# Performance work log

Measured on AMD Instinct MI355X. Metric: run time of the kernel, lower is better.

The kernel has to match this reference:

```python
import jax, jax.numpy as jnp
import numpy as np
import math

B, L1, L2, NHID, NH, HD = 4, 2048, 2048, 1024, 16, 64


def setup_inputs() -> dict:
    key = jax.random.key(0)
    ks = jax.random.split(key, 8)
    s = 1.0 / math.sqrt(NHID)  # keep activations O(1)
    inp1 = jax.random.normal(ks[0], (B, L1, NHID), dtype=jnp.float32)
    inp2 = jax.random.normal(ks[1], (B, L2, NHID), dtype=jnp.float32)
    mask = jnp.zeros((B, L2), dtype=bool)
    Wq = jax.random.normal(ks[2], (NHID, NH * HD), dtype=jnp.float32) * s
    Wk = jax.random.normal(ks[3], (NHID, NH * HD), dtype=jnp.float32) * s
    Wv = jax.random.normal(ks[4], (NHID, NH * HD), dtype=jnp.float32) * s
    Wo = jax.random.normal(ks[5], (NH * HD, NHID), dtype=jnp.float32) * s
    bq = jnp.zeros((NH * HD,), jnp.float32)
    bk = jnp.zeros((NH * HD,), jnp.float32)
    bv = jnp.zeros((NH * HD,), jnp.float32)
    bo = jnp.zeros((NHID,), jnp.float32)
    return dict(inp1=inp1, inp2=inp2, mask=mask, Wq=Wq, bq=bq, Wk=Wk, bk=bk,
                Wv=Wv, bv=bv, Wo=Wo, bo=bo)


def reference(inp1, inp2, mask, Wq, bq, Wk, bk, Wv, bv, Wo, bo):
    # q/k/v projections
    q = (inp1 @ Wq + bq) / math.sqrt(HD)              # [B,L1,NH*HD]
    k = inp2 @ Wk + bk                                 # [B,L2,NH*HD]
    v = inp2 @ Wv + bv                                 # [B,L2,NH*HD]
    q = q.reshape(B, L1, NH, HD)
    k = k.reshape(B, L2, NH, HD)
    v = v.reshape(B, L2, NH, HD)
    # scores [B,NH,L1,L2]
    scores = jnp.einsum('bqhd,bkhd->bhqk', q, k)
    scores = jnp.where(mask[:, None, None, :], jnp.float32(-1e8), scores)
    alpha = jax.nn.softmax(scores, axis=-1)
    attn = jnp.einsum('bhqk,bkhd->bqhd', alpha, v).reshape(B, L1, NH * HD)
    return attn @ Wo + bo                              # [B,L1,NHID]
```

## Files before the change

kernel.cpp:

```cpp
#include <hip/hip_runtime.h>
#include <hip/hip_bf16.h>
#include <stdint.h>

using f32x4  = __attribute__((ext_vector_type(4))) float;
using bf16x8 = __attribute__((ext_vector_type(8))) __bf16;

__device__ __forceinline__ unsigned short f2bf(float f) {
  union { float f; unsigned u; } x; x.f = f;
  unsigned r = x.u + 0x7fffu + ((x.u >> 16) & 1u);
  return (unsigned short)(r >> 16);
}

__device__ __forceinline__ void gload_lds16(const void* g, void* l) {
  __builtin_amdgcn_global_load_lds((const __attribute__((address_space(1))) void*)g,
                                   (__attribute__((address_space(3))) void*)l, 16, 0, 0);
}

__global__ __launch_bounds__(256) void f32_to_bf16_k(const float* __restrict__ in,
                                                     unsigned short* __restrict__ out, int n4) {
  int i = blockIdx.x * 256 + threadIdx.x;
  if (i >= n4) return;
  const float4 v = *(const float4*)(in + (size_t)i * 4);
  union { unsigned short s[4]; uint2 u; } p;
  p.s[0] = f2bf(v.x); p.s[1] = f2bf(v.y); p.s[2] = f2bf(v.z); p.s[3] = f2bf(v.w);
  *(uint2*)(out + (size_t)i * 4) = p.u;
}

__global__ __launch_bounds__(256) void prep_wt_k(const float* __restrict__ W,
                                                 unsigned short* __restrict__ WT, float scale) {
  __shared__ float t[32][33];
  const int tx = threadIdx.x & 31, ty = threadIdx.x >> 5;
  const int gx = blockIdx.x * 32, gy = blockIdx.y * 32;
  #pragma unroll
  for (int r = ty; r < 32; r += 8) t[r][tx] = W[(size_t)(gy + r) * 1024 + gx + tx];
  __syncthreads();
  #pragma unroll
  for (int r = ty; r < 32; r += 8)
    WT[(size_t)(gx + r) * 1024 + gy + tx] = f2bf(t[tx][r] * scale);
}

template<int EPI>
__global__ __launch_bounds__(256) void gemm_bt_k(
    const unsigned short* __restrict__ A,
    const unsigned short* __restrict__ BT,
    const float* __restrict__ bias, float bias_scale,
    void* __restrict__ Cv,
    int M, int N, int K) {
  constexpr int BM = 128, BN = 128, BK = 64;
  __shared__ unsigned short sA[BM * BK];
  __shared__ unsigned short sB[BN * BK];
  const int tid = threadIdx.x;
  const int w = tid >> 6, l = tid & 63, l15 = l & 15, lhi = l >> 4;
  const int wr = w >> 1, wc = w & 1;
  const int m0 = blockIdx.y * BM, n0 = blockIdx.x * BN;

  const f32x4 zero = {0.f, 0.f, 0.f, 0.f};
  f32x4 acc[4][4];
  #pragma unroll
  for (int i = 0; i < 4; i++)
    #pragma unroll
    for (int j = 0; j < 4; j++) acc[i][j] = zero;

  for (int k0 = 0; k0 < K; k0 += BK) {
    __syncthreads();
    #pragma unroll
    for (int i = 0; i < 4; i++) {
      const int p = tid + i * 256;
      const int row = p >> 3;
      const int cl = (p & 7) ^ (row & 7);
      gload_lds16(A + (size_t)(m0 + row) * K + k0 + cl * 8, sA + p * 8);
      gload_lds16(BT + (size_t)(n0 + row) * K + k0 + cl * 8, sB + p * 8);
    }
    __syncthreads();
    #pragma unroll
    for (int kk = 0; kk < 2; kk++) {
      bf16x8 af[4], bfr[4];
      #pragma unroll
      for (int mi = 0; mi < 4; mi++) {
        const int row = wr * 64 + mi * 16 + l15;
        const int c = (kk * 4 + lhi) ^ (row & 7);
        af[mi] = *(const bf16x8*)(sA + row * 64 + c * 8);
      }
      #pragma unroll
      for (int ni = 0; ni < 4; ni++) {
        const int row = wc * 64 + ni * 16 + l15;
        const int c = (kk * 4 + lhi) ^ (row & 7);
        bfr[ni] = *(const bf16x8*)(sB + row * 64 + c * 8);
      }
      #pragma unroll
      for (int mi = 0; mi < 4; mi++)
        #pragma unroll
        for (int ni = 0; ni < 4; ni++)
          acc[mi][ni] = __builtin_amdgcn_mfma_f32_16x16x32_bf16(af[mi], bfr[ni], acc[mi][ni], 0, 0, 0);
    }
  }
  #pragma unroll
  for (int mi = 0; mi < 4; mi++) {
    const int gr = m0 + wr * 64 + mi * 16 + lhi * 4;
    #pragma unroll
    for (int ni = 0; ni < 4; ni++) {
      const int gc = n0 + wc * 64 + ni * 16 + l15;
      const float bs = bias[gc] * bias_scale;
      if constexpr (EPI == 0) {
        unsigned short* C = (unsigned short*)Cv;
        #pragma unroll
        for (int j = 0; j < 4; j++)
          C[(size_t)(gr + j) * N + gc] = f2bf(acc[mi][ni][j] + bs);
      } else if constexpr (EPI == 1) {
        unsigned short* C = (unsigned short*)Cv;
        const int bb = gr >> 11, l2 = gr & 2047;
        const int hh = gc >> 6, dd = gc & 63;
        union { unsigned short s[4]; uint2 u; } pk;
        #pragma unroll
        for (int j = 0; j < 4; j++) pk.s[j] = f2bf(acc[mi][ni][j] + bs);
        *(uint2*)(C + ((size_t)((bb * 16 + hh) * 64 + dd) * 2048 + l2)) = pk.u;
      } else {
        float* C = (float*)Cv;
        #pragma unroll
        for (int j = 0; j < 4; j++)
          C[(size_t)(gr + j) * N + gc] = acc[mi][ni][j] + bs;
      }
    }
  }
}

__global__ __launch_bounds__(256, 3) void flash_k(
    const unsigned short* __restrict__ qb,
    const unsigned short* __restrict__ kb,
    const unsigned short* __restrict__ vTb,
    const unsigned char* __restrict__ mask,
    unsigned short* __restrict__ attnb) {
  __shared__ unsigned short sK[2][64 * 64];
  __shared__ unsigned short sV[2][64 * 64];
  __shared__ unsigned short sP[4][2][16 * 64];
  const int tid = threadIdx.x;
  const int w = tid >> 6, l = tid & 63, l15 = l & 15, lhi = l >> 4;
  const int id = blockIdx.x;
  const int xcd = id & 7;
  const int qt = (id >> 3) & 15;
  const int hb = ((id >> 7) << 3) + xcd;
  const int h = hb & 15, b = hb >> 4;

  const size_t qrowA = (size_t)(b * 2048 + qt * 128 + w * 16 + l15);
  const size_t qrowB = qrowA + 64;
  const bf16x8 aqA0 = *(const bf16x8*)(qb + qrowA * 1024 + h * 64 + lhi * 8);
  const bf16x8 aqA1 = *(const bf16x8*)(qb + qrowA * 1024 + h * 64 + 32 + lhi * 8);
  const bf16x8 aqB0 = *(const bf16x8*)(qb + qrowB * 1024 + h * 64 + lhi * 8);
  const bf16x8 aqB1 = *(const bf16x8*)(qb + qrowB * 1024 + h * 64 + 32 + lhi * 8);

  const f32x4 zero = {0.f, 0.f, 0.f, 0.f};
  f32x4 oaccA[5], oaccB[5];
  #pragma unroll
  for (int d = 0; d < 5; d++) { oaccA[d] = zero; oaccB[d] = zero; }
  float mrowA[4], mrowB[4];
  #pragma unroll
  for (int j = 0; j < 4; j++) { mrowA[j] = 8.0f; mrowB[j] = 8.0f; }

  bf16x8 onef;
  #pragma unroll
  for (int i = 0; i < 8; i++) onef[i] = (__bf16)1.0f;

  const unsigned short* kbase = kb + (size_t)(b * 2048) * 1024 + h * 64;
  const unsigned short* vbase = vTb + (size_t)((b * 16 + h) * 64) * 2048;
  const unsigned char* mbase = mask + b * 2048;
  unsigned short* sPA = sP[w][0];
  unsigned short* sPB = sP[w][1];

  bool anym_lane = false;
  for (int i = l; i < 2048; i += 64) anym_lane |= (mbase[i] != 0);
  const bool anym = __any(anym_lane);

  const int p0 = tid, p1 = tid + 256;
  const int r0 = p0 >> 3, c0s = (p0 & 7) ^ (r0 & 7);
  const int r1 = p1 >> 3, c1s = (p1 & 7) ^ (r1 & 7);
  const unsigned short* kp0 = kbase + (size_t)r0 * 1024 + c0s * 8;
  const unsigned short* kp1 = kbase + (size_t)r1 * 1024 + c1s * 8;
  const unsigned short* vp0 = vbase + (size_t)r0 * 2048 + c0s * 8;
  const unsigned short* vp1 = vbase + (size_t)r1 * 2048 + c1s * 8;

  gload_lds16(kp0, sK[0] + p0 * 8);
  gload_lds16(kp1, sK[0] + p1 * 8);
  gload_lds16(vp0, sV[0] + p0 * 8);
  gload_lds16(vp1, sV[0] + p1 * 8);
  __syncthreads();

  int cur = 0;
  for (int kt = 0; kt < 32; kt++) {
    if (kt < 31) {
      const size_t ko = (size_t)(kt + 1) * 64 * 1024;
      const int vo = (kt + 1) * 64;
      unsigned short* dK = sK[cur ^ 1];
      unsigned short* dV = sV[cur ^ 1];
      gload_lds16(kp0 + ko, dK + p0 * 8);
      gload_lds16(kp1 + ko, dK + p1 * 8);
      gload_lds16(vp0 + vo, dV + p0 * 8);
      gload_lds16(vp1 + vo, dV + p1 * 8);
    }
    const unsigned short* cK = sK[cur];
    const unsigned short* cV = sV[cur];

    f32x4 sA[4], sB[4];
    #pragma unroll
    for (int n = 0; n < 4; n++) { sA[n] = zero; sB[n] = zero; }
    #pragma unroll
    for (int n = 0; n < 4; n++) {
      const int row = n * 16 + l15;
      const int cc0 = lhi ^ (row & 7);
      const int cc1 = (4 + lhi) ^ (row & 7);
      const bf16x8 k0 = *(const bf16x8*)(cK + row * 64 + cc0 * 8);
      const bf16x8 k1 = *(const bf16x8*)(cK + row * 64 + cc1 * 8);
      sA[n] = __builtin_amdgcn_mfma_f32_16x16x32_bf16(aqA0, k0, sA[n], 0, 0, 0);
      sA[n] = __builtin_amdgcn_mfma_f32_16x16x32_bf16(aqA1, k1, sA[n], 0, 0, 0);
      sB[n] = __builtin_amdgcn_mfma_f32_16x16x32_bf16(aqB0, k0, sB[n], 0, 0, 0);
      sB[n] = __builtin_amdgcn_mfma_f32_16x16x32_bf16(aqB1, k1, sB[n], 0, 0, 0);
    }

    if (anym) {
      #pragma unroll
      for (int n = 0; n < 4; n++) {
        const float mb = mbase[kt * 64 + n * 16 + l15] ? -1e8f : 0.f;
        #pragma unroll
        for (int j = 0; j < 4; j++) { sA[n][j] += mb; sB[n][j] += mb; }
      }
    }

    {
      float lmax[4];
      #pragma unroll
      for (int j = 0; j < 4; j++)
        lmax[j] = fmaxf(fmaxf(sA[0][j], sA[1][j]), fmaxf(sA[2][j], sA[3][j]));
      const bool need = (lmax[0] > mrowA[0]) | (lmax[1] > mrowA[1]) |
                        (lmax[2] > mrowA[2]) | (lmax[3] > mrowA[3]);
      if (__any(need)) {
        float tmax[4] = {lmax[0], lmax[1], lmax[2], lmax[3]};
        #pragma unroll
        for (int d = 1; d < 16; d <<= 1)
          #pragma unroll
          for (int j = 0; j < 4; j++) tmax[j] = fmaxf(tmax[j], __shfl_xor(tmax[j], d));
        #pragma unroll
        for (int j = 0; j < 4; j++) {
          const float mnew = fmaxf(mrowA[j], tmax[j]);
          const float scl = exp2f(mrowA[j] - mnew);
          mrowA[j] = mnew;
          #pragma unroll
          for (int d = 0; d < 5; d++) oaccA[d][j] *= scl;
        }
      }
    }
    {
      float lmax[4];
      #pragma unroll
      for (int j = 0; j < 4; j++)
        lmax[j] = fmaxf(fmaxf(sB[0][j], sB[1][j]), fmaxf(sB[2][j], sB[3][j]));
      const bool need = (lmax[0] > mrowB[0]) | (lmax[1] > mrowB[1]) |
                        (lmax[2] > mrowB[2]) | (lmax[3] > mrowB[3]);
      if (__any(need)) {
        float tmax[4] = {lmax[0], lmax[1], lmax[2], lmax[3]};
        #pragma unroll
        for (int d = 1; d < 16; d <<= 1)
          #pragma unroll
          for (int j = 0; j < 4; j++) tmax[j] = fmaxf(tmax[j], __shfl_xor(tmax[j], d));
        #pragma unroll
        for (int j = 0; j < 4; j++) {
          const float mnew = fmaxf(mrowB[j], tmax[j]);
          const float scl = exp2f(mrowB[j] - mnew);
          mrowB[j] = mnew;
          #pragma unroll
          for (int d = 0; d < 5; d++) oaccB[d][j] *= scl;
        }
      }
    }

    #pragma unroll
    for (int n = 0; n < 4; n++)
      #pragma unroll
      for (int j = 0; j < 4; j++) {
        const int row = lhi * 4 + j;
        const int col = n * 16 + l15;
        const int cc = (col >> 3) ^ (row & 7);
        *(__bf16*)(sPA + row * 64 + cc * 8 + (col & 7)) = (__bf16)exp2f(sA[n][j] - mrowA[j]);
        *(__bf16*)(sPB + row * 64 + cc * 8 + (col & 7)) = (__bf16)exp2f(sB[n][j] - mrowB[j]);
      }
    asm volatile("s_waitcnt lgkmcnt(0)" ::: "memory");
    __builtin_amdgcn_sched_barrier(0);
    {
      const int prow = l15;
      const int pc0 = lhi ^ (prow & 7);
      const int pc1 = (4 + lhi) ^ (prow & 7);
      const bf16x8 paA0 = *(const bf16x8*)(sPA + prow * 64 + pc0 * 8);
      const bf16x8 paA1 = *(const bf16x8*)(sPA + prow * 64 + pc1 * 8);
      const bf16x8 paB0 = *(const bf16x8*)(sPB + prow * 64 + pc0 * 8);
      const bf16x8 paB1 = *(const bf16x8*)(sPB + prow * 64 + pc1 * 8);
      #pragma unroll
      for (int df = 0; df < 4; df++) {
        const int row = df * 16 + l15;
        const int cc0 = lhi ^ (row & 7);
        const int cc1 = (4 + lhi) ^ (row & 7);
        const bf16x8 v0 = *(const bf16x8*)(cV + row * 64 + cc0 * 8);
        const bf16x8 v1 = *(const bf16x8*)(cV + row * 64 + cc1 * 8);
        oaccA[df] = __builtin_amdgcn_mfma_f32_16x16x32_bf16(paA0, v0, oaccA[df], 0, 0, 0);
        oaccA[df] = __builtin_amdgcn_mfma_f32_16x16x32_bf16(paA1, v1, oaccA[df], 0, 0, 0);
        oaccB[df] = __builtin_amdgcn_mfma_f32_16x16x32_bf16(paB0, v0, oaccB[df], 0, 0, 0);
        oaccB[df] = __builtin_amdgcn_mfma_f32_16x16x32_bf16(paB1, v1, oaccB[df], 0, 0, 0);
      }
      oaccA[4] = __builtin_amdgcn_mfma_f32_16x16x32_bf16(paA0, onef, oaccA[4], 0, 0, 0);
      oaccA[4] = __builtin_amdgcn_mfma_f32_16x16x32_bf16(paA1, onef, oaccA[4], 0, 0, 0);
      oaccB[4] = __builtin_amdgcn_mfma_f32_16x16x32_bf16(paB0, onef, oaccB[4], 0, 0, 0);
      oaccB[4] = __builtin_amdgcn_mfma_f32_16x16x32_bf16(paB1, onef, oaccB[4], 0, 0, 0);
    }
    __syncthreads();
    cur ^= 1;
  }

  float invA[4], invB[4];
  #pragma unroll
  for (int j = 0; j < 4; j++) { invA[j] = 1.0f / oaccA[4][j]; invB[j] = 1.0f / oaccB[4][j]; }
  #pragma unroll
  for (int df = 0; df < 4; df++)
    #pragma unroll
    for (int j = 0; j < 4; j++) {
      const size_t rA = (size_t)(b * 2048 + qt * 128 + w * 16 + lhi * 4 + j);
      attnb[rA * 1024 + h * 64 + df * 16 + l15] = f2bf(oaccA[df][j] * invA[j]);
      attnb[(rA + 64) * 1024 + h * 64 + df * 16 + l15] = f2bf(oaccB[df][j] * invB[j]);
    }
}

extern "C" void kernel_launch(void* const* d_in, const int* in_sizes, int n_in,
                              void* d_out, int out_size, void* d_ws, size_t ws_size,
                              hipStream_t stream) {
  (void)in_sizes; (void)n_in; (void)out_size; (void)ws_size;
  const float* inp1 = (const float*)d_in[0];
  const float* inp2 = (const float*)d_in[1];
  const unsigned char* mask = (const unsigned char*)d_in[2];
  const float* Wq = (const float*)d_in[3];
  const float* bq = (const float*)d_in[4];
  const float* Wk = (const float*)d_in[5];
  const float* bk = (const float*)d_in[6];
  const float* Wv = (const float*)d_in[7];
  const float* bv = (const float*)d_in[8];
  const float* Wo = (const float*)d_in[9];
  const float* bo = (const float*)d_in[10];
  float* out = (float*)d_out;

  char* p = (char*)d_ws;
  auto alloc = [&](size_t bytes) { char* r = p; p += (bytes + 255) & ~(size_t)255; return r; };
  const size_t ACT = 8192ull * 1024 * 2;
  const size_t WSZ = 1024ull * 1024 * 2;
  unsigned short* x1b  = (unsigned short*)alloc(ACT);
  unsigned short* x2b  = (unsigned short*)alloc(ACT);
  unsigned short* WqT  = (unsigned short*)alloc(WSZ);
  unsigned short* WkT  = (unsigned short*)alloc(WSZ);
  unsigned short* WvT  = (unsigned short*)alloc(WSZ);
  unsigned short* WoT  = (unsigned short*)alloc(WSZ);
  unsigned short* qbuf = (unsigned short*)alloc(ACT);
  unsigned short* kbuf = (unsigned short*)alloc(ACT);
  unsigned short* vTbf = (unsigned short*)alloc(ACT);
  unsigned short* attb = x1b;

  const float QS = 0.18033688011112042f;

  f32_to_bf16_k<<<8192, 256, 0, stream>>>(inp1, x1b, 2097152);
  f32_to_bf16_k<<<8192, 256, 0, stream>>>(inp2, x2b, 2097152);
  dim3 tg(32, 32);
  prep_wt_k<<<tg, 256, 0, stream>>>(Wq, WqT, QS);
  prep_wt_k<<<tg, 256, 0, stream>>>(Wk, WkT, 1.f);
  prep_wt_k<<<tg, 256, 0, stream>>>(Wv, WvT, 1.f);
  prep_wt_k<<<tg, 256, 0, stream>>>(Wo, WoT, 1.f);
  dim3 gg(8, 64);
  gemm_bt_k<0><<<gg, 256, 0, stream>>>(x1b, WqT, bq, QS, qbuf, 8192, 1024, 1024);
  gemm_bt_k<0><<<gg, 256, 0, stream>>>(x2b, WkT, bk, 1.f, kbuf, 8192, 1024, 1024);
  gemm_bt_k<1><<<gg, 256, 0, stream>>>(x2b, WvT, bv, 1.f, vTbf, 8192, 1024, 1024);
  flash_k<<<1024, 256, 0, stream>>>(qbuf, kbuf, vTbf, mask, attb);
  gemm_bt_k<2><<<gg, 256, 0, stream>>>(attb, WoT, bo, 1.f, out, 8192, 1024, 1024);
}
```

Measured before the change: 276.4 us.

## Fuse K/V projection GEMMs, merge input conversions, and halve flash P scratch

The two input f32-to-bf16 conversion launches become one kernel, and the K and V projection GEMMs become a single N=2048 GEMM whose epilogue writes K row-major and V transposed. In the flash kernel, the per-wave P scratch is cut to one 16x64 buffer that the two 16-row halves reuse in turn, and occupancy is raised from 3 to 4 blocks per CU. s_setprio hints are placed around the MFMA sections. The aim is fewer launches, better reuse of the x2 activation, and more waves in flight. The cost is that the two PV passes are now serialized through one shared buffer, and register pressure is higher under the tighter launch bound.

```diff
diff --git a/kernel.cpp b/kernel.cpp
--- a/kernel.cpp
+++ b/kernel.cpp
@@ -16,14 +16,18 @@
                                    (__attribute__((address_space(3))) void*)l, 16, 0, 0);
 }
 
-__global__ __launch_bounds__(256) void f32_to_bf16_k(const float* __restrict__ in,
-                                                     unsigned short* __restrict__ out, int n4) {
+__global__ __launch_bounds__(256) void conv_in_k(const float* __restrict__ in1,
+                                                 const float* __restrict__ in2,
+                                                 unsigned short* __restrict__ o1,
+                                                 unsigned short* __restrict__ o2) {
   int i = blockIdx.x * 256 + threadIdx.x;
-  if (i >= n4) return;
-  const float4 v = *(const float4*)(in + (size_t)i * 4);
+  const float* in = in1; unsigned short* o = o1;
+  int k = i;
+  if (i >= 2097152) { in = in2; o = o2; k = i - 2097152; }
+  const float4 v = *(const float4*)(in + (size_t)k * 4);
   union { unsigned short s[4]; uint2 u; } p;
   p.s[0] = f2bf(v.x); p.s[1] = f2bf(v.y); p.s[2] = f2bf(v.z); p.s[3] = f2bf(v.w);
-  *(uint2*)(out + (size_t)i * 4) = p.u;
+  *(uint2*)(o + (size_t)k * 4) = p.u;
 }
 
 __global__ __launch_bounds__(256) void prep_wt_k(const float* __restrict__ W,
@@ -43,8 +47,8 @@
 __global__ __launch_bounds__(256) void gemm_bt_k(
     const unsigned short* __restrict__ A,
     const unsigned short* __restrict__ BT,
-    const float* __restrict__ bias, float bias_scale,
-    void* __restrict__ Cv,
+    const float* __restrict__ bias, const float* __restrict__ bias2, float bias_scale,
+    void* __restrict__ Cv, void* __restrict__ Cv2,
     int M, int N, int K) {
   constexpr int BM = 128, BN = 128, BK = 64;
   __shared__ unsigned short sA[BM * BK];
@@ -100,31 +104,42 @@
     #pragma unroll
     for (int ni = 0; ni < 4; ni++) {
       const int gc = n0 + wc * 64 + ni * 16 + l15;
-      const float bs = bias[gc] * bias_scale;
       if constexpr (EPI == 0) {
+        const float bs = bias[gc] * bias_scale;
         unsigned short* C = (unsigned short*)Cv;
         #pragma unroll
         for (int j = 0; j < 4; j++)
           C[(size_t)(gr + j) * N + gc] = f2bf(acc[mi][ni][j] + bs);
-      } else if constexpr (EPI == 1) {
-        unsigned short* C = (unsigned short*)Cv;
-        const int bb = gr >> 11, l2 = gr & 2047;
-        const int hh = gc >> 6, dd = gc & 63;
-        union { unsigned short s[4]; uint2 u; } pk;
-        #pragma unroll
-        for (int j = 0; j < 4; j++) pk.s[j] = f2bf(acc[mi][ni][j] + bs);
-        *(uint2*)(C + ((size_t)((bb * 16 + hh) * 64 + dd) * 2048 + l2)) = pk.u;
-      } else {
+      } else if constexpr (EPI == 2) {
+        const float bs = bias[gc] * bias_scale;
         float* C = (float*)Cv;
         #pragma unroll
         for (int j = 0; j < 4; j++)
           C[(size_t)(gr + j) * N + gc] = acc[mi][ni][j] + bs;
+      } else {
+        if (n0 < 1024) {
+          const float bs = bias[gc];
+          unsigned short* C = (unsigned short*)Cv;
+          #pragma unroll
+          for (int j = 0; j < 4; j++)
+            C[(size_t)(gr + j) * 1024 + gc] = f2bf(acc[mi][ni][j] + bs);
+        } else {
+          const int gc2 = gc - 1024;
+          const float bs = bias2[gc2];
+          unsigned short* C = (unsigned short*)Cv2;
+          const int bb = gr >> 11, l2 = gr & 2047;
+          const int hh = gc2 >> 6, dd = gc2 & 63;
+          union { unsigned short s[4]; uint2 u; } pk;
+          #pragma unroll
+          for (int j = 0; j < 4; j++) pk.s[j] = f2bf(acc[mi][ni][j] + bs);
+          *(uint2*)(C + ((size_t)((bb * 16 + hh) * 64 + dd) * 2048 + l2)) = pk.u;
+        }
       }
     }
   }
 }
 
-__global__ __launch_bounds__(256, 3) void flash_k(
+__global__ __launch_bounds__(256, 4) void flash_k(
     const unsigned short* __restrict__ qb,
     const unsigned short* __restrict__ kb,
     const unsigned short* __restrict__ vTb,
@@ -132,7 +147,7 @@
     unsigned short* __restrict__ attnb) {
   __shared__ unsigned short sK[2][64 * 64];
   __shared__ unsigned short sV[2][64 * 64];
-  __shared__ unsigned short sP[4][2][16 * 64];
+  __shared__ unsigned short sP[4][16 * 64];
   const int tid = threadIdx.x;
   const int w = tid >> 6, l = tid & 63, l15 = l & 15, lhi = l >> 4;
   const int id = blockIdx.x;
@@ -163,8 +178,7 @@
   const unsigned short* kbase = kb + (size_t)(b * 2048) * 1024 + h * 64;
   const unsigned short* vbase = vTb + (size_t)((b * 16 + h) * 64) * 2048;
   const unsigned char* mbase = mask + b * 2048;
-  unsigned short* sPA = sP[w][0];
-  unsigned short* sPB = sP[w][1];
+  unsigned short* sPw = sP[w];
 
   bool anym_lane = false;
   for (int i = l; i < 2048; i += 64) anym_lane |= (mbase[i] != 0);
@@ -202,6 +216,7 @@
     f32x4 sA[4], sB[4];
     #pragma unroll
     for (int n = 0; n < 4; n++) { sA[n] = zero; sB[n] = zero; }
+    __builtin_amdgcn_s_setprio(1);
     #pragma unroll
     for (int n = 0; n < 4; n++) {
       const int row = n * 16 + l15;
@@ -214,6 +229,7 @@
       sB[n] = __builtin_amdgcn_mfma_f32_16x16x32_bf16(aqB0, k0, sB[n], 0, 0, 0);
       sB[n] = __builtin_amdgcn_mfma_f32_16x16x32_bf16(aqB1, k1, sB[n], 0, 0, 0);
     }
+    __builtin_amdgcn_s_setprio(0);
 
     if (anym) {
       #pragma unroll
@@ -271,6 +287,12 @@
       }
     }
 
+    f32x4 eB[4];
+    #pragma unroll
+    for (int n = 0; n < 4; n++)
+      #pragma unroll
+      for (int j = 0; j < 4; j++) eB[n][j] = exp2f(sB[n][j] - mrowB[j]);
+
     #pragma unroll
     for (int n = 0; n < 4; n++)
       #pragma unroll
@@ -278,8 +300,7 @@
         const int row = lhi * 4 + j;
         const int col = n * 16 + l15;
         const int cc = (col >> 3) ^ (row & 7);
-        *(__bf16*)(sPA + row * 64 + cc * 8 + (col & 7)) = (__bf16)exp2f(sA[n][j] - mrowA[j]);
-        *(__bf16*)(sPB + row * 64 + cc * 8 + (col & 7)) = (__bf16)exp2f(sB[n][j] - mrowB[j]);
+        *(__bf16*)(sPw + row * 64 + cc * 8 + (col & 7)) = (__bf16)exp2f(sA[n][j] - mrowA[j]);
       }
     asm volatile("s_waitcnt lgkmcnt(0)" ::: "memory");
     __builtin_amdgcn_sched_barrier(0);
@@ -287,10 +308,9 @@
       const int prow = l15;
       const int pc0 = lhi ^ (prow & 7);
       const int pc1 = (4 + lhi) ^ (prow & 7);
-      const bf16x8 paA0 = *(const bf16x8*)(sPA + prow * 64 + pc0 * 8);
-      const bf16x8 paA1 = *(const bf16x8*)(sPA + prow * 64 + pc1 * 8);
-      const bf16x8 paB0 = *(const bf16x8*)(sPB + prow * 64 + pc0 * 8);
-      const bf16x8 paB1 = *(const bf16x8*)(sPB + prow * 64 + pc1 * 8);
+      const bf16x8 paA0 = *(const bf16x8*)(sPw + prow * 64 + pc0 * 8);
+      const bf16x8 paA1 = *(const bf16x8*)(sPw + prow * 64 + pc1 * 8);
+      __builtin_amdgcn_s_setprio(1);
       #pragma unroll
       for (int df = 0; df < 4; df++) {
         const int row = df * 16 + l15;
@@ -300,13 +320,43 @@
         const bf16x8 v1 = *(const bf16x8*)(cV + row * 64 + cc1 * 8);
         oaccA[df] = __builtin_amdgcn_mfma_f32_16x16x32_bf16(paA0, v0, oaccA[df], 0, 0, 0);
         oaccA[df] = __builtin_amdgcn_mfma_f32_16x16x32_bf16(paA1, v1, oaccA[df], 0, 0, 0);
+      }
+      oaccA[4] = __builtin_amdgcn_mfma_f32_16x16x32_bf16(paA0, onef, oaccA[4], 0, 0, 0);
+      oaccA[4] = __builtin_amdgcn_mfma_f32_16x16x32_bf16(paA1, onef, oaccA[4], 0, 0, 0);
+      __builtin_amdgcn_s_setprio(0);
+    }
+
+    #pragma unroll
+    for (int n = 0; n < 4; n++)
+      #pragma unroll
+      for (int j = 0; j < 4; j++) {
+        const int row = lhi * 4 + j;
+        const int col = n * 16 + l15;
+        const int cc = (col >> 3) ^ (row & 7);
+        *(__bf16*)(sPw + row * 64 + cc * 8 + (col & 7)) = (__bf16)eB[n][j];
+      }
+    asm volatile("s_waitcnt lgkmcnt(0)" ::: "memory");
+    __builtin_amdgcn_sched_barrier(0);
+    {
+      const int prow = l15;
+      const int pc0 = lhi ^ (prow & 7);
+      const int pc1 = (4 + lhi) ^ (prow & 7);
+      const bf16x8 paB0 = *(const bf16x8*)(sPw + prow * 64 + pc0 * 8);
+      const bf16x8 paB1 = *(const bf16x8*)(sPw + prow * 64 + pc1 * 8);
+      __builtin_amdgcn_s_setprio(1);
+      #pragma unroll
+      for (int df = 0; df < 4; df++) {
+        const int row = df * 16 + l15;
+        const int cc0 = lhi ^ (row & 7);
+        const int cc1 = (4 + lhi) ^ (row & 7);
+        const bf16x8 v0 = *(const bf16x8*)(cV + row * 64 + cc0 * 8);
+        const bf16x8 v1 = *(const bf16x8*)(cV + row * 64 + cc1 * 8);
         oaccB[df] = __builtin_amdgcn_mfma_f32_16x16x32_bf16(paB0, v0, oaccB[df], 0, 0, 0);
         oaccB[df] = __builtin_amdgcn_mfma_f32_16x16x32_bf16(paB1, v1, oaccB[df], 0, 0, 0);
       }
-      oaccA[4] = __builtin_amdgcn_mfma_f32_16x16x32_bf16(paA0, onef, oaccA[4], 0, 0, 0);
-      oaccA[4] = __builtin_amdgcn_mfma_f32_16x16x32_bf16(paA1, onef, oaccA[4], 0, 0, 0);
       oaccB[4] = __builtin_amdgcn_mfma_f32_16x16x32_bf16(paB0, onef, oaccB[4], 0, 0, 0);
       oaccB[4] = __builtin_amdgcn_mfma_f32_16x16x32_bf16(paB1, onef, oaccB[4], 0, 0, 0);
+      __builtin_amdgcn_s_setprio(0);
     }
     __syncthreads();
     cur ^= 1;
@@ -349,8 +399,7 @@
   unsigned short* x1b  = (unsigned short*)alloc(ACT);
   unsigned short* x2b  = (unsigned short*)alloc(ACT);
   unsigned short* WqT  = (unsigned short*)alloc(WSZ);
-  unsigned short* WkT  = (unsigned short*)alloc(WSZ);
-  unsigned short* WvT  = (unsigned short*)alloc(WSZ);
+  unsigned short* WkvT = (unsigned short*)alloc(2 * WSZ);
   unsigned short* WoT  = (unsigned short*)alloc(WSZ);
   unsigned short* qbuf = (unsigned short*)alloc(ACT);
   unsigned short* kbuf = (unsigned short*)alloc(ACT);
@@ -359,17 +408,14 @@
 
   const float QS = 0.18033688011112042f;
 
-  f32_to_bf16_k<<<8192, 256, 0, stream>>>(inp1, x1b, 2097152);
-  f32_to_bf16_k<<<8192, 256, 0, stream>>>(inp2, x2b, 2097152);
+  conv_in_k<<<16384, 256, 0, stream>>>(inp1, inp2, x1b, x2b);
   dim3 tg(32, 32);
   prep_wt_k<<<tg, 256, 0, stream>>>(Wq, WqT, QS);
-  prep_wt_k<<<tg, 256, 0, stream>>>(Wk, WkT, 1.f);
-  prep_wt_k<<<tg, 256, 0, stream>>>(Wv, WvT, 1.f);
+  prep_wt_k<<<tg, 256, 0, stream>>>(Wk, WkvT, 1.f);
+  prep_wt_k<<<tg, 256, 0, stream>>>(Wv, WkvT + 1024 * 1024, 1.f);
   prep_wt_k<<<tg, 256, 0, stream>>>(Wo, WoT, 1.f);
-  dim3 gg(8, 64);
-  gemm_bt_k<0><<<gg, 256, 0, stream>>>(x1b, WqT, bq, QS, qbuf, 8192, 1024, 1024);
-  gemm_bt_k<0><<<gg, 256, 0, stream>>>(x2b, WkT, bk, 1.f, kbuf, 8192, 1024, 1024);
-  gemm_bt_k<1><<<gg, 256, 0, stream>>>(x2b, WvT, bv, 1.f, vTbf, 8192, 1024, 1024);
+  gemm_bt_k<0><<<dim3(8, 64), 256, 0, stream>>>(x1b, WqT, bq, nullptr, QS, qbuf, nullptr, 8192, 1024, 1024);
+  gemm_bt_k<3><<<dim3(16, 64), 256, 0, stream>>>(x2b, WkvT, bk, bv, 1.f, kbuf, vTbf, 8192, 2048, 1024);
   flash_k<<<1024, 256, 0, stream>>>(qbuf, kbuf, vTbf, mask, attb);
-  gemm_bt_k<2><<<gg, 256, 0, stream>>>(attb, WoT, bo, 1.f, out, 8192, 1024, 1024);
-}
+  gemm_bt_k<2><<<dim3(8, 64), 256, 0, stream>>>(attb, WoT, bo, nullptr, 1.f, out, nullptr, 8192, 1024, 1024);
+}
```

Measured after the change: 306.5 us. 1.11x slower.
